# Optimization experiments

Hardware: AMD Instinct MI355X
Metric: run time of the kernel (lower is better)

## Reference

```python
import jax, jax.numpy as jnp
import numpy as np

N_HEAD = 16
N_EMBD = 1024
B, T = 4, 1024


def setup_inputs() -> dict:
    key = jax.random.key(0)
    ks = jax.random.split(key, 8)
    hs = N_EMBD // N_HEAD
    x = jax.random.normal(ks[0], (B, T, N_EMBD), dtype=jnp.float32)
    # previous-layer attention load per token, ~O(1/T) like a softmax column mean
    refractory_state = jax.random.uniform(ks[1], (B, T), dtype=jnp.float32) / T
    s_attn = 1.0 / np.sqrt(N_EMBD)
    W_attn = jax.random.normal(ks[2], (N_EMBD, 3 * N_EMBD), dtype=jnp.float32) * s_attn
    b_attn = jnp.zeros((3 * N_EMBD,), dtype=jnp.float32)
    W_proj = jax.random.normal(ks[3], (N_EMBD, N_EMBD), dtype=jnp.float32) * s_attn
    b_proj = jnp.zeros((N_EMBD,), dtype=jnp.float32)
    # learnable LIF params, init per module (lif_mode='refractory')
    threshold = jnp.full((N_HEAD,), 0.01, dtype=jnp.float32)
    leak = jnp.full((N_HEAD,), 2.0, dtype=jnp.float32)
    steepness = jnp.full((N_HEAD,), 2.0, dtype=jnp.float32)
    ref_strength = jnp.full((N_HEAD,), -2.0, dtype=jnp.float32)
    cross_w = jnp.full((N_HEAD,), -2.0, dtype=jnp.float32)
    return {
        "x": x, "refractory_state": refractory_state,
        "W_attn": W_attn, "b_attn": b_attn,
        "W_proj": W_proj, "b_proj": b_proj,
        "threshold": threshold, "leak": leak, "steepness": steepness,
        "ref_strength": ref_strength, "cross_w": cross_w,
    }


def reference(x, refractory_state, W_attn, b_attn, W_proj, b_proj,
              threshold, leak, steepness, ref_strength, cross_w):
    Bq, Tq, C = x.shape
    H = N_HEAD
    hs = C // H
    qkv = x @ W_attn + b_attn                     # [B,T,3C]
    q, k, v = jnp.split(qkv, 3, axis=-1)
    q = q.reshape(Bq, Tq, H, hs).transpose(0, 2, 1, 3)  # [B,H,T,hs]
    k = k.reshape(Bq, Tq, H, hs).transpose(0, 2, 1, 3)
    v = v.reshape(Bq, Tq, H, hs).transpose(0, 2, 1, 3)

    att = jnp.einsum('bhqd,bhkd->bhqk', q, k) * (1.0 / jnp.sqrt(jnp.asarray(hs, x.dtype)))
    causal = jnp.tril(jnp.ones((Tq, Tq), dtype=bool))
    att = jnp.where(causal[None, None], att, -jnp.inf)
    probs = jax.nn.softmax(att, axis=-1)          # [B,H,T,T]

    thr = (jnp.abs(threshold) * 0.1)[None, :, None, None]
    lk = jax.nn.sigmoid(leak)[None, :, None, None]
    st = jax.nn.softplus(steepness)[None, :, None, None]
    # refractory: column load over queries + cross-layer load
    column_load = probs.mean(axis=-2, keepdims=True)          # [B,H,1,T]
    eff_thr = thr + jax.nn.softplus(ref_strength)[None, :, None, None] * column_load
    eff_thr = eff_thr + jax.nn.sigmoid(cross_w)[None, :, None, None] * refractory_state[:, None, None, :]

    fire = jax.nn.sigmoid(st * (probs - eff_thr))
    lif_w = fire + lk * (1.0 - fire)
    mod = probs * lif_w
    mod = mod / (mod.sum(axis=-1, keepdims=True) + 1e-8)
    new_refractory = mod.mean(axis=1).mean(axis=-2)           # [B,T]

    y = jnp.einsum('bhqk,bhkd->bhqd', mod, v)
    y = y.transpose(0, 2, 1, 3).reshape(Bq, Tq, C)
    y = y @ W_proj + b_proj
    return y, new_refractory
```

## Files before the change

### kernel.cpp

```cpp
#include <hip/hip_runtime.h>
#include <math.h>

#define B_  4
#define T_  1024
#define C_  1024
#define H_  16
#define HS_ 64
#define K2E 0.1803368801f
#define LOG2E 1.44269504f

typedef _Float16 f16;
typedef _Float16 f16x8 __attribute__((ext_vector_type(8)));
typedef _Float16 f16x4 __attribute__((ext_vector_type(4)));
typedef float f32x4 __attribute__((ext_vector_type(4)));

#define MFMA16(a,b,c) __builtin_amdgcn_mfma_f32_16x16x32_f16(a,b,c,0,0,0)
#define EXP2(x) __builtin_amdgcn_exp2f(x)
#define RCP(x)  __builtin_amdgcn_rcpf(x)

#define PSTRIDE_BH 557056

__device__ __forceinline__ float qsum_(float v){
    v += __shfl_xor(v,1,64); v += __shfl_xor(v,2,64);
    v += __shfl_xor(v,4,64); v += __shfl_xor(v,8,64);
    return v;
}
__device__ __forceinline__ float sigmoidf_(float x){ return 1.0f/(1.0f + __expf(-x)); }
__device__ __forceinline__ float softplusf_(float x){ return fmaxf(x, 0.0f) + log1pf(__expf(-fabsf(x))); }

__device__ __forceinline__ void gload_lds16(const f16* g, f16* l){
    __builtin_amdgcn_global_load_lds(
        (__attribute__((address_space(1))) void*)(void*)g,
        (__attribute__((address_space(3))) void*)(void*)l, 16, 0, 0);
}

__global__ __launch_bounds__(256) void prep_k(
    const float* __restrict__ x, const float* __restrict__ Wa,
    const float* __restrict__ Wp,
    f16* __restrict__ x_h, f16* __restrict__ WaT, f16* __restrict__ WpT,
    float* __restrict__ zbase)
{
    __shared__ float tl[32][33];
    const int bid = blockIdx.x, tid = threadIdx.x;
    if (bid < 2048){
        int i = bid*256 + tid;
        const float4* p = (const float4*)x + (size_t)i*2;
        float4 a = p[0], b = p[1];
        f16x8 o;
        o[0]=(f16)a.x; o[1]=(f16)a.y; o[2]=(f16)a.z; o[3]=(f16)a.w;
        o[4]=(f16)b.x; o[5]=(f16)b.y; o[6]=(f16)b.z; o[7]=(f16)b.w;
        *((f16x8*)x_h + i) = o;
    } else if (bid < 5120){
        int t = bid - 2048;
        int n0 = (t % 96)*32, k0 = (t / 96)*32;
        const int c = tid & 31, r4 = tid >> 5;
        #pragma unroll
        for (int i=0;i<4;i++){ int r = r4*4+i; tl[r][c] = Wa[(size_t)(k0+r)*3072 + n0 + c]; }
        __syncthreads();
        #pragma unroll
        for (int i=0;i<4;i++){ int r = r4*4+i; WaT[(size_t)(n0+r)*1024 + k0 + c] = (f16)tl[c][r]; }
    } else if (bid < 6144){
        int t = bid - 5120;
        int n0 = (t & 31)*32, k0 = (t >> 5)*32;
        const int c = tid & 31, r4 = tid >> 5;
        #pragma unroll
        for (int i=0;i<4;i++){ int r = r4*4+i; tl[r][c] = Wp[(size_t)(k0+r)*1024 + n0 + c]; }
        __syncthreads();
        #pragma unroll
        for (int i=0;i<4;i++){ int r = r4*4+i; WpT[(size_t)(n0+r)*1024 + k0 + c] = (f16)tl[c][r]; }
    } else {
        int idx = (bid - 6144)*256 + tid;
        float4 z; z.x=0.f; z.y=0.f; z.z=0.f; z.w=0.f;
        ((float4*)zbase)[idx] = z;
    }
}

#define CT_STRIDE 132
__global__ __launch_bounds__(256) void gemm_qkv_k(
    const f16* __restrict__ A, const f16* __restrict__ Bt,
    const float* __restrict__ bias,
    f16* __restrict__ Qh, f16* __restrict__ Kh, f16* __restrict__ Vt)
{
    __shared__ __align__(16) f16 smem[16896];
    const int tid = threadIdx.x;
    const int lane = tid & 63, wave = tid >> 6;
    const int lx = lane & 15, quad = lane >> 4;
    const int wm = wave & 1, wn = wave >> 1;
    const int lin = blockIdx.y*24 + blockIdx.x;
    const int nb  = (lin & 7)*96 + (lin >> 3);
    const int m0 = (nb/24)*128, n0 = (nb%24)*128;
    const f16* Ap = A  + (size_t)m0*1024;
    const f16* Bp = Bt + (size_t)n0*1024;
    f32x4 acc[4][4];
    #pragma unroll
    for (int i=0;i<4;i++){
        #pragma unroll
        for (int j=0;j<4;j++){ acc[i][j][0]=0.f;acc[i][j][1]=0.f;acc[i][j][2]=0.f;acc[i][j][3]=0.f; }
    }
#define GQ_STAGE(BUF, KT) { \
    const int k0s = (KT)*32; \
    for (int i=0;i<2;i++){ int c=i*4+wave; \
        gload_lds16(Ap + (size_t)(c*16+lx)*1024 + k0s + quad*8, &smem[(BUF) + c*512]); \
        gload_lds16(Bp + (size_t)(c*16+lx)*1024 + k0s + quad*8, &smem[(BUF) + 4096 + c*512]); } }
#define GQ_COMP(BUF) { \
    f16x8 af[4], bf[4]; \
    for (int mt=0;mt<4;mt++) af[mt] = *(const f16x8*)&smem[(BUF) + (wm*4+mt)*512 + quad*128 + lx*8]; \
    for (int nt=0;nt<4;nt++) bf[nt] = *(const f16x8*)&smem[(BUF) + 4096 + (wn*4+nt)*512 + quad*128 + lx*8]; \
    for (int mt=0;mt<4;mt++) \
        for (int nt=0;nt<4;nt++) \
            acc[mt][nt] = MFMA16(af[mt], bf[nt], acc[mt][nt]); }

    GQ_STAGE(0, 0);
    __syncthreads();
    #pragma unroll 1
    for (int it=0; it<32; it+=2){
        if (it+1 < 32) GQ_STAGE(8192, it+1);
        GQ_COMP(0);
        __syncthreads();
        if (it+2 < 32) GQ_STAGE(0, it+2);
        GQ_COMP(8192);
        __syncthreads();
    }
    f16* Ct = smem;
    #pragma unroll
    for (int mt=0;mt<4;mt++){
        #pragma unroll
        for (int nt=0;nt<4;nt++){
            int n_loc = wn*64 + nt*16 + lx;
            float bv = bias[n0 + n_loc];
            #pragma unroll
            for (int r=0;r<4;r++){
                int m_loc = wm*64 + mt*16 + quad*4 + r;
                Ct[m_loc*CT_STRIDE + n_loc] = (f16)(acc[mt][nt][r] + bv);
            }
        }
    }
    __syncthreads();
    const int bb = m0 >> 10;
    if (n0 < 2048){
        for (int it=0; it<8; it++){
            int row = it*32 + wave*8 + (lane>>3);
            int ch  = lane & 7;
            int m_loc = row >> 1, half = row & 1;
            f16x8 v = *(const f16x8*)&Ct[m_loc*CT_STRIDE + half*64 + ch*8];
            int n = n0 + half*64;
            int which = n >> 10, cc = n & 1023, h = cc >> 6;
            int t = (m0 + m_loc) & 1023;
            f16* dst = (which==0) ? Qh : Kh;
            *(f16x8*)(dst + ((size_t)(bb*16+h)*1024 + t)*64 + ch*8) = v;
        }
    } else {
        for (int it=0; it<8; it++){
            int drow = it*16 + wave*4 + (lane>>4);
            int ch   = lane & 15;
            int cc = (n0 + drow) & 1023;
            int h = cc >> 6, d = cc & 63;
            f16 tmp[8];
            #pragma unroll
            for (int j=0;j<8;j++) tmp[j] = Ct[(ch*8+j)*CT_STRIDE + drow];
            int t = (m0 + ch*8) & 1023;
            *(f16x8*)(Vt + ((size_t)(bb*16+h)*64 + d)*1024 + t) = *(f16x8*)tmp;
        }
    }
}

__global__ __launch_bounds__(256) void gemm_proj_k(
    const f16* __restrict__ A, const f16* __restrict__ Bt,
    const float* __restrict__ bias, float* __restrict__ out,
    const float* __restrict__ racc)
{
    if (blockIdx.x == 512){
        float* oref = out + (size_t)B_*T_*C_;
        #pragma unroll
        for (int j=0;j<16;j++){
            int idx = j*256 + threadIdx.x;
            oref[idx] = racc[idx] * (1.0f/(H_*T_));
        }
        return;
    }
    __shared__ __align__(16) f16 smem[12288];
    const int tid = threadIdx.x;
    const int lane = tid & 63, wave = tid >> 6;
    const int lx = lane & 15, quad = lane >> 4;
    const int wm = wave & 1, wn = wave >> 1;
    const int lin = blockIdx.x;
    const int nb  = (lin & 7)*64 + (lin >> 3);
    const int m0 = (nb >> 4)*128, n0 = (nb & 15)*64;
    const f16* Ap = A  + (size_t)m0*1024;
    const f16* Bp = Bt + (size_t)n0*1024;
    f32x4 acc[4][2];
    #pragma unroll
    for (int i=0;i<4;i++){
        #pragma unroll
        for (int j=0;j<2;j++){ acc[i][j][0]=0.f;acc[i][j][1]=0.f;acc[i][j][2]=0.f;acc[i][j][3]=0.f; }
    }
#define GP_STAGE(BUF, KT) { \
    const int k0s = (KT)*32; \
    for (int i=0;i<2;i++){ int c=i*4+wave; \
        gload_lds16(Ap + (size_t)(c*16+lx)*1024 + k0s + quad*8, &smem[(BUF) + c*512]); } \
    gload_lds16(Bp + (size_t)(wave*16+lx)*1024 + k0s + quad*8, &smem[(BUF) + 4096 + wave*512]); }
#define GP_COMP(BUF) { \
    f16x8 af[4], bf[2]; \
    for (int mt=0;mt<4;mt++) af[mt] = *(const f16x8*)&smem[(BUF) + (wm*4+mt)*512 + quad*128 + lx*8]; \
    for (int nt=0;nt<2;nt++) bf[nt] = *(const f16x8*)&smem[(BUF) + 4096 + (wn*2+nt)*512 + quad*128 + lx*8]; \
    for (int mt=0;mt<4;mt++) \
        for (int nt=0;nt<2;nt++) \
            acc[mt][nt] = MFMA16(af[mt], bf[nt], acc[mt][nt]); }

    GP_STAGE(0, 0);
    __syncthreads();
    #pragma unroll 1
    for (int it=0; it<32; it+=2){
        if (it+1 < 32) GP_STAGE(6144, it+1);
        GP_COMP(0);
        __syncthreads();
        if (it+2 < 32) GP_STAGE(0, it+2);
        GP_COMP(6144);
        __syncthreads();
    }
    #pragma unroll
    for (int mt=0;mt<4;mt++){
        #pragma unroll
        for (int nt=0;nt<2;nt++){
            int n = n0 + wn*32 + nt*16 + lx;
            float bv = bias[n];
            #pragma unroll
            for (int r=0;r<4;r++){
                int m = m0 + wm*64 + mt*16 + quad*4 + r;
                out[(size_t)m*1024 + n] = acc[mt][nt][r] + bv;
            }
        }
    }
}

__global__ __launch_bounds__(256) void attn_stats_k(
    const f16* __restrict__ Qh, const f16* __restrict__ Kh,
    float* __restrict__ rowl, float* __restrict__ colp,
    f16* __restrict__ Pbuf)
{
    __shared__ __align__(16) f16 Kl[8192];
    __shared__ __align__(16) f16 Pl[4][16*72];
    __shared__ float invl_sh[64];
    const int tid = threadIdx.x;
    const int lane = tid & 63, wave = tid >> 6;
    const int lx = lane & 15, quad = lane >> 4;
    const int j  = blockIdx.x >> 6;
    const int bh = blockIdx.x & 63;
    const int qpos = wave*16 + quad*4;
    const size_t kbase = (size_t)bh*65536;

#define KLOAD(dst, KT) { \
    for (int i=0;i<2;i++){ int u=i*4+wave, cc=u&3, kh=u>>2; \
        dst[i] = *(const f16x8*)(Kh + kbase + (size_t)((KT)*64 + cc*16+lx)*64 + kh*32 + quad*8); } }
#define KSTORE(src, BUF) { \
    for (int i=0;i<2;i++){ int u=i*4+wave, cc=u&3, kh=u>>2; \
        *(f16x8*)&Kl[(BUF) + cc*1024 + kh*512 + quad*128 + lx*8] = src[i]; } }
#define STATS1_TILE(KT, BUF) { \
    const bool diag = ((KT) == g); \
    for (int nt=0;nt<4;nt++){ \
        f32x4 sc = {0.f,0.f,0.f,0.f}; \
        f16x8 b0 = *(const f16x8*)&Kl[(BUF) + nt*1024 + quad*128 + lx*8]; \
        f16x8 b1 = *(const f16x8*)&Kl[(BUF) + nt*1024 + 512 + quad*128 + lx*8]; \
        sc = MFMA16(aq0, b0, sc); \
        sc = MFMA16(aq1, b1, sc); \
        for (int r=0;r<4;r++){ \
            float sv = sc[r]; \
            if (diag && (nt*16+lx) > (qpos + r)) sv = -1e4f; \
            float p = EXP2(sv*K2E); \
            ls[r] += p; \
            Pl[wave][(quad*4+r)*72 + nt*16 + lx] = (f16)p; \
        } } \
    for (int it2=0; it2<2; it2++){ \
        int qq = it2*8 + (lane>>3), chh = lane & 7; \
        f16x8 v = *(const f16x8*)&Pl[wave][qq*72 + chh*8]; \
        *(f16x8*)(Pblk + (size_t)(wave*16+qq)*S + (KT)*64 + chh*8) = v; } }

    #pragma unroll 1
    for (int pass=0; pass<2; ++pass){
        const int g = pass ? j : (15 - j);
        const int S = (g+1)*64;
        f16* __restrict__ Pblk = Pbuf + (size_t)bh*PSTRIDE_BH + (size_t)4096*((g*(g+1))>>1);
        const size_t qoff = ((size_t)bh*1024 + g*64 + wave*16 + lx)*64;
        f16x8 aq0 = *(const f16x8*)(Qh + qoff + quad*8);
        f16x8 aq1 = *(const f16x8*)(Qh + qoff + 32 + quad*8);

        f16x8 rkE[2], rkO[2];
        float ls[4] = {0.f,0.f,0.f,0.f};
        KLOAD(rkE, 0);
        KSTORE(rkE, 0);
        if (g >= 1) KLOAD(rkO, 1);
        __syncthreads();
        #pragma unroll 1
        for (int kt=0; kt<=g; kt+=2){
            if (kt+2 <= g) KLOAD(rkE, kt+2);
            if (kt+1 <= g) KSTORE(rkO, 4096);
            STATS1_TILE(kt, 0);
            __syncthreads();
            if (kt+1 <= g){
                if (kt+3 <= g) KLOAD(rkO, kt+3);
                if (kt+2 <= g) KSTORE(rkE, 0);
                STATS1_TILE(kt+1, 4096);
                __syncthreads();
            }
        }
        #pragma unroll
        for (int r=0;r<4;r++){
            float l = qsum_(ls[r]);
            if (lx == 0){
                rowl[(size_t)bh*1024 + g*64 + qpos + r] = l;
                invl_sh[qpos + r] = RCP(l);
            }
        }
        __syncthreads();
        if (tid < (g+1)*16){
            const int k0 = tid*4;
            float a0=0.f, a1=0.f, a2=0.f, a3=0.f;
            const f16* pr = Pblk + k0;
            #pragma unroll 4
            for (int q=0;q<64;q++){
                f16x4 v = *(const f16x4*)(pr + (size_t)q*S);
                float w = invl_sh[q];
                a0 += (float)v[0]*w; a1 += (float)v[1]*w;
                a2 += (float)v[2]*w; a3 += (float)v[3]*w;
            }
            float* cp = colp + (size_t)bh*1024 + k0;
            atomicAdd(cp+0,a0); atomicAdd(cp+1,a1);
            atomicAdd(cp+2,a2); atomicAdd(cp+3,a3);
        }
    }
}

__global__ __launch_bounds__(256) void attn_apply_k(
    const f16* __restrict__ Vt,
    const float* __restrict__ rowl,
    const float* __restrict__ colp, const float* __restrict__ refr,
    const float* __restrict__ threshold, const float* __restrict__ leak,
    const float* __restrict__ steepness, const float* __restrict__ ref_strength,
    const float* __restrict__ cross_w,
    f16* __restrict__ Yh, float* __restrict__ racc,
    f16* __restrict__ Pbuf)
{
    __shared__ __align__(16) f16 Vl[8192];
    __shared__ __align__(16) f16 Pl[4][16*72];
    __shared__ float eb[1024];
    __shared__ float invl_sh[64];
    __shared__ float invD_sh[64];
    const int tid = threadIdx.x;
    const int lane = tid & 63, wave = tid >> 6;
    const int lx = lane & 15, quad = lane >> 4;
    const int qr8 = lane >> 3, c8 = lane & 7;
    const int j  = blockIdx.x >> 6;
    const int bh = blockIdx.x & 63;
    const int b  = bh >> 4, h = bh & 15;
    const size_t kbase = (size_t)bh*65536;

    const float thr = fabsf(threshold[h])*0.1f;
    const float lk  = sigmoidf_(leak[h]);
    const float st2 = softplusf_(steepness[h]) * LOG2E;
    const float sprT= softplusf_(ref_strength[h]) * (1.0f/T_);
    const float cw  = sigmoidf_(cross_w[h]);
    const float Alk = 1.f - lk;

    {
        float4 cp = *(const float4*)(colp + (size_t)bh*1024 + tid*4);
        float4 rf = *(const float4*)(refr + (size_t)b*1024 + tid*4);
        eb[tid*4+0] = st2*(thr + sprT*cp.x + cw*rf.x);
        eb[tid*4+1] = st2*(thr + sprT*cp.y + cw*rf.y);
        eb[tid*4+2] = st2*(thr + sprT*cp.z + cw*rf.z);
        eb[tid*4+3] = st2*(thr + sprT*cp.w + cw*rf.w);
    }

#define VLOAD(dst, KT) { \
    for (int i=0;i<2;i++){ int u=i*4+wave, cc=u&3, kh=u>>2; \
        dst[i] = *(const f16x8*)(Vt + kbase + (size_t)(cc*16+lx)*1024 + (KT)*64 + kh*32 + quad*8); } }
#define VSTORE(src, BUF) { \
    for (int i=0;i<2;i++){ int u=i*4+wave, cc=u&3, kh=u>>2; \
        *(f16x8*)&Vl[(BUF) + cc*1024 + kh*512 + quad*128 + lx*8] = src[i]; } }
#define PLOAD(dst, KT) { \
    dst[0] = *(const f16x8*)(Pblk + (size_t)(wave*16 + qr8)*S + (KT)*64 + c8*8); \
    dst[1] = *(const f16x8*)(Pblk + (size_t)(wave*16 + 8 + qr8)*S + (KT)*64 + c8*8); }
#define APPLY1_TILE(KT, BUF, pv) { \
    float ebv[8]; \
    *(float4*)&ebv[0] = *(const float4*)&eb[(KT)*64 + c8*8]; \
    *(float4*)&ebv[4] = *(const float4*)&eb[(KT)*64 + c8*8 + 4]; \
    f16x8 o0, o1; \
    for (int jj=0;jj<8;jj++){ \
        float pj = (float)pv[0][jj] * w0; \
        float fire = RCP(1.f + EXP2(ebv[jj] - st2*pj)); \
        float pw = pj*(lk + Alk*fire); \
        Dp0 += pw; o0[jj] = (f16)pw; } \
    for (int jj=0;jj<8;jj++){ \
        float pj = (float)pv[1][jj] * w1; \
        float fire = RCP(1.f + EXP2(ebv[jj] - st2*pj)); \
        float pw = pj*(lk + Alk*fire); \
        Dp1 += pw; o1[jj] = (f16)pw; } \
    *(f16x8*)&Pl[wave][qr8*72 + c8*8] = o0; \
    *(f16x8*)&Pl[wave][(8+qr8)*72 + c8*8] = o1; \
    { f16x8 ap0 = *(const f16x8*)&Pl[wave][lx*72 + quad*8]; \
      f16x8 ap1 = *(const f16x8*)&Pl[wave][lx*72 + 32 + quad*8]; \
      for (int dt=0;dt<4;dt++){ \
        f16x8 bv0 = *(const f16x8*)&Vl[(BUF) + dt*1024 + quad*128 + lx*8]; \
        f16x8 bv1 = *(const f16x8*)&Vl[(BUF) + dt*1024 + 512 + quad*128 + lx*8]; \
        y[dt] = MFMA16(ap0, bv0, y[dt]); \
        y[dt] = MFMA16(ap1, bv1, y[dt]); } } }

    #pragma unroll 1
    for (int pass=0; pass<2; ++pass){
        const int g = pass ? j : (15 - j);
        const int S = (g+1)*64;
        f16* __restrict__ Pblk = Pbuf + (size_t)bh*PSTRIDE_BH + (size_t)4096*((g*(g+1))>>1);

        __syncthreads();
        if (tid < 64) invl_sh[tid] = RCP(rowl[(size_t)bh*1024 + g*64 + tid]);
        __syncthreads();

        const float w0 = invl_sh[wave*16 + qr8];
        const float w1 = invl_sh[wave*16 + 8 + qr8];

        f32x4 y[4];
        #pragma unroll
        for (int i=0;i<4;i++){ y[i][0]=0.f;y[i][1]=0.f;y[i][2]=0.f;y[i][3]=0.f; }
        float Dp0 = 0.f, Dp1 = 0.f;

        f16x8 rvE[2], rvO[2], pvE[2], pvO[2];
        VLOAD(rvE, 0); PLOAD(pvE, 0);
        VSTORE(rvE, 0);
        if (g >= 1){ VLOAD(rvO, 1); PLOAD(pvO, 1); }
        __syncthreads();
        #pragma unroll 1
        for (int kt=0; kt<=g; kt+=2){
            if (kt+2 <= g) VLOAD(rvE, kt+2);
            if (kt+1 <= g) VSTORE(rvO, 4096);
            APPLY1_TILE(kt, 0, pvE);
            if (kt+2 <= g) PLOAD(pvE, kt+2);
            __syncthreads();
            if (kt+1 <= g){
                if (kt+3 <= g) VLOAD(rvO, kt+3);
                if (kt+2 <= g) VSTORE(rvE, 0);
                APPLY1_TILE(kt+1, 4096, pvO);
                if (kt+3 <= g) PLOAD(pvO, kt+3);
                __syncthreads();
            }
        }
        Dp0 += __shfl_xor(Dp0,1,64); Dp0 += __shfl_xor(Dp0,2,64); Dp0 += __shfl_xor(Dp0,4,64);
        Dp1 += __shfl_xor(Dp1,1,64); Dp1 += __shfl_xor(Dp1,2,64); Dp1 += __shfl_xor(Dp1,4,64);
        if (c8 == 0){
            invD_sh[wave*16 + qr8]     = RCP(Dp0 + 1e-8f);
            invD_sh[wave*16 + 8 + qr8] = RCP(Dp1 + 1e-8f);
        }
        __syncthreads();

        float invD[4];
        #pragma unroll
        for (int r=0;r<4;r++) invD[r] = invD_sh[wave*16 + quad*4 + r];
        #pragma unroll
        for (int dt=0;dt<4;dt++){
            #pragma unroll
            for (int r=0;r<4;r++)
                Pl[wave][(quad*4+r)*72 + dt*16 + lx] = (f16)(y[dt][r]*invD[r]);
        }
        #pragma unroll
        for (int it=0; it<2; it++){
            int q = it*8 + (lane>>3), ch = lane & 7;
            f16x8 v = *(const f16x8*)&Pl[wave][q*72 + ch*8];
            *(f16x8*)(Yh + (size_t)(b*1024 + g*64 + wave*16 + q)*1024 + h*64 + ch*8) = v;
        }

        if (tid < (g+1)*16){
            const int k0 = tid*4;
            float4 ebv = *(const float4*)&eb[k0];
            float a0=0.f, a1=0.f, a2=0.f, a3=0.f;
            const f16* pr = Pblk + k0;
            #pragma unroll 4
            for (int q=0;q<64;q++){
                f16x4 v = *(const f16x4*)(pr + (size_t)q*S);
                float wl = invl_sh[q], wd = invD_sh[q];
                float p0 = (float)v[0]*wl, p1 = (float)v[1]*wl;
                float p2 = (float)v[2]*wl, p3 = (float)v[3]*wl;
                float f0 = RCP(1.f + EXP2(ebv.x - st2*p0));
                float f1 = RCP(1.f + EXP2(ebv.y - st2*p1));
                float f2 = RCP(1.f + EXP2(ebv.z - st2*p2));
                float f3 = RCP(1.f + EXP2(ebv.w - st2*p3));
                a0 += p0*(lk + Alk*f0)*wd; a1 += p1*(lk + Alk*f1)*wd;
                a2 += p2*(lk + Alk*f2)*wd; a3 += p3*(lk + Alk*f3)*wd;
            }
            float* rp = racc + (size_t)b*1024 + k0;
            atomicAdd(rp+0,a0); atomicAdd(rp+1,a1);
            atomicAdd(rp+2,a2); atomicAdd(rp+3,a3);
        }
    }
}

extern "C" void kernel_launch(void* const* d_in, const int* in_sizes, int n_in,
                              void* d_out, int out_size, void* d_ws, size_t ws_size,
                              hipStream_t stream) {
    (void)in_sizes; (void)n_in; (void)out_size; (void)ws_size;
    const float* x           = (const float*)d_in[0];
    const float* refr        = (const float*)d_in[1];
    const float* W_attn      = (const float*)d_in[2];
    const float* b_attn      = (const float*)d_in[3];
    const float* W_proj      = (const float*)d_in[4];
    const float* b_proj      = (const float*)d_in[5];
    const float* threshold   = (const float*)d_in[6];
    const float* leak        = (const float*)d_in[7];
    const float* steepness   = (const float*)d_in[8];
    const float* ref_strength= (const float*)d_in[9];
    const float* cross_w     = (const float*)d_in[10];
    float* out = (float*)d_out;

    char* ws = (char*)d_ws;
    f16* x_h = (f16*)ws;                       ws += (size_t)4096*1024*2;
    f16* WaT = (f16*)ws;                       ws += (size_t)3072*1024*2;
    f16* WpT = (f16*)ws;                       ws += (size_t)1024*1024*2;
    f16* Qh  = (f16*)ws;                       ws += (size_t)64*1024*64*2;
    f16* Kh  = (f16*)ws;                       ws += (size_t)64*1024*64*2;
    f16* Vt  = (f16*)ws;                       ws += (size_t)64*64*1024*2;
    f16* Yh  = (f16*)ws;                       ws += (size_t)4096*1024*2;
    float* rowl = (float*)ws;                  ws += (size_t)65536*4;
    float* colp = (float*)ws;                  ws += (size_t)65536*4;
    float* racc = (float*)ws;                  ws += (size_t)4096*4;
    f16* Pbuf = (f16*)ws;                      ws += (size_t)64*PSTRIDE_BH*2;

    prep_k<<<dim3(6212), dim3(256), 0, stream>>>(x, W_attn, W_proj, x_h, WaT, WpT, colp);
    gemm_qkv_k<<<dim3(24,32), dim3(256), 0, stream>>>(x_h, WaT, b_attn, Qh, Kh, Vt);
    attn_stats_k<<<dim3(512), dim3(256), 0, stream>>>(Qh, Kh, rowl, colp, Pbuf);
    attn_apply_k<<<dim3(512), dim3(256), 0, stream>>>(
        Vt, rowl, colp, refr,
        threshold, leak, steepness, ref_strength, cross_w, Yh, racc, Pbuf);
    gemm_proj_k<<<dim3(513), dim3(256), 0, stream>>>(Yh, WpT, b_proj, out, racc);
}
```

Baseline: 268.8 us.

## Split paired query tiles into separate blocks and load K/V directly into registers

Both attention kernels used to process two query tiles per block (g and 15-g) to balance causal work. Now each block handles a single tile, with twice as many blocks launched, ordered so the heaviest tiles start first. The K and V tiles are no longer staged through shared memory. Each wave loads its MFMA B operands straight from global memory into registers, which removes the LDS stores and most __syncthreads in the main loops. The cost is redundant global and L2 reads across the four waves, more registers, and reliance on block scheduling for load balance.

```diff
diff --git a/kernel.cpp b/kernel.cpp
--- a/kernel.cpp
+++ b/kernel.cpp
@@ -238,31 +238,33 @@
     float* __restrict__ rowl, float* __restrict__ colp,
     f16* __restrict__ Pbuf)
 {
-    __shared__ __align__(16) f16 Kl[8192];
     __shared__ __align__(16) f16 Pl[4][16*72];
     __shared__ float invl_sh[64];
     const int tid = threadIdx.x;
     const int lane = tid & 63, wave = tid >> 6;
     const int lx = lane & 15, quad = lane >> 4;
-    const int j  = blockIdx.x >> 6;
+    const int g  = 15 - (blockIdx.x >> 6);
     const int bh = blockIdx.x & 63;
     const int qpos = wave*16 + quad*4;
     const size_t kbase = (size_t)bh*65536;
-
-#define KLOAD(dst, KT) { \
-    for (int i=0;i<2;i++){ int u=i*4+wave, cc=u&3, kh=u>>2; \
-        dst[i] = *(const f16x8*)(Kh + kbase + (size_t)((KT)*64 + cc*16+lx)*64 + kh*32 + quad*8); } }
-#define KSTORE(src, BUF) { \
-    for (int i=0;i<2;i++){ int u=i*4+wave, cc=u&3, kh=u>>2; \
-        *(f16x8*)&Kl[(BUF) + cc*1024 + kh*512 + quad*128 + lx*8] = src[i]; } }
-#define STATS1_TILE(KT, BUF) { \
+    const int S = (g+1)*64;
+    f16* __restrict__ Pblk = Pbuf + (size_t)bh*PSTRIDE_BH + (size_t)4096*((g*(g+1))>>1);
+
+    const size_t qoff = ((size_t)bh*1024 + g*64 + wave*16 + lx)*64;
+    f16x8 aq0 = *(const f16x8*)(Qh + qoff + quad*8);
+    f16x8 aq1 = *(const f16x8*)(Qh + qoff + 32 + quad*8);
+
+#define KLOADX(dst, KT) { \
+    for (int nt=0;nt<4;nt++){ \
+        const f16* kp = Kh + kbase + (size_t)((KT)*64 + nt*16 + lx)*64 + quad*8; \
+        dst[nt*2]   = *(const f16x8*)(kp); \
+        dst[nt*2+1] = *(const f16x8*)(kp + 32); } }
+#define STATS_TILE(KT, rk) { \
     const bool diag = ((KT) == g); \
     for (int nt=0;nt<4;nt++){ \
         f32x4 sc = {0.f,0.f,0.f,0.f}; \
-        f16x8 b0 = *(const f16x8*)&Kl[(BUF) + nt*1024 + quad*128 + lx*8]; \
-        f16x8 b1 = *(const f16x8*)&Kl[(BUF) + nt*1024 + 512 + quad*128 + lx*8]; \
-        sc = MFMA16(aq0, b0, sc); \
-        sc = MFMA16(aq1, b1, sc); \
+        sc = MFMA16(aq0, rk[nt*2],   sc); \
+        sc = MFMA16(aq1, rk[nt*2+1], sc); \
         for (int r=0;r<4;r++){ \
             float sv = sc[r]; \
             if (diag && (nt*16+lx) > (qpos + r)) sv = -1e4f; \
@@ -275,58 +277,42 @@
         f16x8 v = *(const f16x8*)&Pl[wave][qq*72 + chh*8]; \
         *(f16x8*)(Pblk + (size_t)(wave*16+qq)*S + (KT)*64 + chh*8) = v; } }
 
+    f16x8 rkE[8], rkO[8];
+    float ls[4] = {0.f,0.f,0.f,0.f};
+    KLOADX(rkE, 0);
+    if (g >= 1) KLOADX(rkO, 1);
     #pragma unroll 1
-    for (int pass=0; pass<2; ++pass){
-        const int g = pass ? j : (15 - j);
-        const int S = (g+1)*64;
-        f16* __restrict__ Pblk = Pbuf + (size_t)bh*PSTRIDE_BH + (size_t)4096*((g*(g+1))>>1);
-        const size_t qoff = ((size_t)bh*1024 + g*64 + wave*16 + lx)*64;
-        f16x8 aq0 = *(const f16x8*)(Qh + qoff + quad*8);
-        f16x8 aq1 = *(const f16x8*)(Qh + qoff + 32 + quad*8);
-
-        f16x8 rkE[2], rkO[2];
-        float ls[4] = {0.f,0.f,0.f,0.f};
-        KLOAD(rkE, 0);
-        KSTORE(rkE, 0);
-        if (g >= 1) KLOAD(rkO, 1);
-        __syncthreads();
-        #pragma unroll 1
-        for (int kt=0; kt<=g; kt+=2){
-            if (kt+2 <= g) KLOAD(rkE, kt+2);
-            if (kt+1 <= g) KSTORE(rkO, 4096);
-            STATS1_TILE(kt, 0);
-            __syncthreads();
-            if (kt+1 <= g){
-                if (kt+3 <= g) KLOAD(rkO, kt+3);
-                if (kt+2 <= g) KSTORE(rkE, 0);
-                STATS1_TILE(kt+1, 4096);
-                __syncthreads();
-            }
-        }
-        #pragma unroll
-        for (int r=0;r<4;r++){
-            float l = qsum_(ls[r]);
-            if (lx == 0){
-                rowl[(size_t)bh*1024 + g*64 + qpos + r] = l;
-                invl_sh[qpos + r] = RCP(l);
-            }
-        }
-        __syncthreads();
-        if (tid < (g+1)*16){
-            const int k0 = tid*4;
-            float a0=0.f, a1=0.f, a2=0.f, a3=0.f;
-            const f16* pr = Pblk + k0;
-            #pragma unroll 4
-            for (int q=0;q<64;q++){
-                f16x4 v = *(const f16x4*)(pr + (size_t)q*S);
-                float w = invl_sh[q];
-                a0 += (float)v[0]*w; a1 += (float)v[1]*w;
-                a2 += (float)v[2]*w; a3 += (float)v[3]*w;
-            }
-            float* cp = colp + (size_t)bh*1024 + k0;
-            atomicAdd(cp+0,a0); atomicAdd(cp+1,a1);
-            atomicAdd(cp+2,a2); atomicAdd(cp+3,a3);
-        }
+    for (int kt=0; kt<=g; kt+=2){
+        STATS_TILE(kt, rkE);
+        if (kt+2 <= g) KLOADX(rkE, kt+2);
+        if (kt+1 <= g){
+            STATS_TILE(kt+1, rkO);
+            if (kt+3 <= g) KLOADX(rkO, kt+3);
+        }
+    }
+    #pragma unroll
+    for (int r=0;r<4;r++){
+        float l = qsum_(ls[r]);
+        if (lx == 0){
+            rowl[(size_t)bh*1024 + g*64 + qpos + r] = l;
+            invl_sh[qpos + r] = RCP(l);
+        }
+    }
+    __syncthreads();
+    if (tid < (g+1)*16){
+        const int k0 = tid*4;
+        float a0=0.f, a1=0.f, a2=0.f, a3=0.f;
+        const f16* pr = Pblk + k0;
+        #pragma unroll 4
+        for (int q=0;q<64;q++){
+            f16x4 v = *(const f16x4*)(pr + (size_t)q*S);
+            float w = invl_sh[q];
+            a0 += (float)v[0]*w; a1 += (float)v[1]*w;
+            a2 += (float)v[2]*w; a3 += (float)v[3]*w;
+        }
+        float* cp = colp + (size_t)bh*1024 + k0;
+        atomicAdd(cp+0,a0); atomicAdd(cp+1,a1);
+        atomicAdd(cp+2,a2); atomicAdd(cp+3,a3);
     }
 }
 
@@ -340,7 +326,6 @@
     f16* __restrict__ Yh, float* __restrict__ racc,
     f16* __restrict__ Pbuf)
 {
-    __shared__ __align__(16) f16 Vl[8192];
     __shared__ __align__(16) f16 Pl[4][16*72];
     __shared__ float eb[1024];
     __shared__ float invl_sh[64];
@@ -348,11 +333,12 @@
     const int tid = threadIdx.x;
     const int lane = tid & 63, wave = tid >> 6;
     const int lx = lane & 15, quad = lane >> 4;
-    const int qr8 = lane >> 3, c8 = lane & 7;
-    const int j  = blockIdx.x >> 6;
+    const int g  = 15 - (blockIdx.x >> 6);
     const int bh = blockIdx.x & 63;
     const int b  = bh >> 4, h = bh & 15;
     const size_t kbase = (size_t)bh*65536;
+    const int S = (g+1)*64;
+    f16* __restrict__ Pblk = Pbuf + (size_t)bh*PSTRIDE_BH + (size_t)4096*((g*(g+1))>>1);
 
     const float thr = fabsf(threshold[h])*0.1f;
     const float lk  = sigmoidf_(leak[h]);
@@ -369,125 +355,107 @@
         eb[tid*4+2] = st2*(thr + sprT*cp.z + cw*rf.z);
         eb[tid*4+3] = st2*(thr + sprT*cp.w + cw*rf.w);
     }
-
-#define VLOAD(dst, KT) { \
-    for (int i=0;i<2;i++){ int u=i*4+wave, cc=u&3, kh=u>>2; \
-        dst[i] = *(const f16x8*)(Vt + kbase + (size_t)(cc*16+lx)*1024 + (KT)*64 + kh*32 + quad*8); } }
-#define VSTORE(src, BUF) { \
-    for (int i=0;i<2;i++){ int u=i*4+wave, cc=u&3, kh=u>>2; \
-        *(f16x8*)&Vl[(BUF) + cc*1024 + kh*512 + quad*128 + lx*8] = src[i]; } }
-#define PLOAD(dst, KT) { \
-    dst[0] = *(const f16x8*)(Pblk + (size_t)(wave*16 + qr8)*S + (KT)*64 + c8*8); \
-    dst[1] = *(const f16x8*)(Pblk + (size_t)(wave*16 + 8 + qr8)*S + (KT)*64 + c8*8); }
-#define APPLY1_TILE(KT, BUF, pv) { \
-    float ebv[8]; \
-    *(float4*)&ebv[0] = *(const float4*)&eb[(KT)*64 + c8*8]; \
-    *(float4*)&ebv[4] = *(const float4*)&eb[(KT)*64 + c8*8 + 4]; \
-    f16x8 o0, o1; \
+    if (tid < 64) invl_sh[tid] = RCP(rowl[(size_t)bh*1024 + g*64 + tid]);
+    __syncthreads();
+
+    const float wli = invl_sh[wave*16 + lx];
+
+    f32x4 y[4];
+    #pragma unroll
+    for (int i=0;i<4;i++){ y[i][0]=0.f;y[i][1]=0.f;y[i][2]=0.f;y[i][3]=0.f; }
+    float Dp = 0.f;
+
+#define PLOADX(dst, KT) { \
+    const f16* pp = Pblk + (size_t)(wave*16 + lx)*S + (KT)*64 + quad*8; \
+    dst[0] = *(const f16x8*)(pp); \
+    dst[1] = *(const f16x8*)(pp + 32); }
+#define RVLOAD(dst, KT) { \
+    for (int dt=0;dt<4;dt++){ \
+        const f16* vp = Vt + kbase + (size_t)(dt*16 + lx)*1024 + (KT)*64 + quad*8; \
+        dst[dt*2]   = *(const f16x8*)(vp); \
+        dst[dt*2+1] = *(const f16x8*)(vp + 32); } }
+#define LIF_TILE(KT, pv, af0, af1) { \
+    const float* ebp = &eb[(KT)*64 + quad*8]; \
+    float4 eA0 = *(const float4*)(ebp); \
+    float4 eA1 = *(const float4*)(ebp+4); \
+    float4 eB0 = *(const float4*)(ebp+32); \
+    float4 eB1 = *(const float4*)(ebp+36); \
+    float ea[8] = {eA0.x,eA0.y,eA0.z,eA0.w,eA1.x,eA1.y,eA1.z,eA1.w}; \
+    float ebb[8] = {eB0.x,eB0.y,eB0.z,eB0.w,eB1.x,eB1.y,eB1.z,eB1.w}; \
     for (int jj=0;jj<8;jj++){ \
-        float pj = (float)pv[0][jj] * w0; \
-        float fire = RCP(1.f + EXP2(ebv[jj] - st2*pj)); \
-        float pw = pj*(lk + Alk*fire); \
-        Dp0 += pw; o0[jj] = (f16)pw; } \
+        float p = (float)pv[0][jj] * wli; \
+        float fire = RCP(1.f + EXP2(ea[jj] - st2*p)); \
+        float pw = p*(lk + Alk*fire); \
+        Dp += pw; af0[jj] = (f16)pw; } \
     for (int jj=0;jj<8;jj++){ \
-        float pj = (float)pv[1][jj] * w1; \
-        float fire = RCP(1.f + EXP2(ebv[jj] - st2*pj)); \
-        float pw = pj*(lk + Alk*fire); \
-        Dp1 += pw; o1[jj] = (f16)pw; } \
-    *(f16x8*)&Pl[wave][qr8*72 + c8*8] = o0; \
-    *(f16x8*)&Pl[wave][(8+qr8)*72 + c8*8] = o1; \
-    { f16x8 ap0 = *(const f16x8*)&Pl[wave][lx*72 + quad*8]; \
-      f16x8 ap1 = *(const f16x8*)&Pl[wave][lx*72 + 32 + quad*8]; \
-      for (int dt=0;dt<4;dt++){ \
-        f16x8 bv0 = *(const f16x8*)&Vl[(BUF) + dt*1024 + quad*128 + lx*8]; \
-        f16x8 bv1 = *(const f16x8*)&Vl[(BUF) + dt*1024 + 512 + quad*128 + lx*8]; \
-        y[dt] = MFMA16(ap0, bv0, y[dt]); \
-        y[dt] = MFMA16(ap1, bv1, y[dt]); } } }
-
+        float p = (float)pv[1][jj] * wli; \
+        float fire = RCP(1.f + EXP2(ebb[jj] - st2*p)); \
+        float pw = p*(lk + Alk*fire); \
+        Dp += pw; af1[jj] = (f16)pw; } }
+#define MFMA8(af0, af1, rv) { \
+    for (int dt=0;dt<4;dt++){ \
+        y[dt] = MFMA16(af0, rv[dt*2],   y[dt]); \
+        y[dt] = MFMA16(af1, rv[dt*2+1], y[dt]); } }
+
+    f16x8 rv[8], pvE[2], pvO[2], af0, af1;
+    PLOADX(pvE, 0);
+    if (g >= 1) PLOADX(pvO, 1);
     #pragma unroll 1
-    for (int pass=0; pass<2; ++pass){
-        const int g = pass ? j : (15 - j);
-        const int S = (g+1)*64;
-        f16* __restrict__ Pblk = Pbuf + (size_t)bh*PSTRIDE_BH + (size_t)4096*((g*(g+1))>>1);
-
-        __syncthreads();
-        if (tid < 64) invl_sh[tid] = RCP(rowl[(size_t)bh*1024 + g*64 + tid]);
-        __syncthreads();
-
-        const float w0 = invl_sh[wave*16 + qr8];
-        const float w1 = invl_sh[wave*16 + 8 + qr8];
-
-        f32x4 y[4];
-        #pragma unroll
-        for (int i=0;i<4;i++){ y[i][0]=0.f;y[i][1]=0.f;y[i][2]=0.f;y[i][3]=0.f; }
-        float Dp0 = 0.f, Dp1 = 0.f;
-
-        f16x8 rvE[2], rvO[2], pvE[2], pvO[2];
-        VLOAD(rvE, 0); PLOAD(pvE, 0);
-        VSTORE(rvE, 0);
-        if (g >= 1){ VLOAD(rvO, 1); PLOAD(pvO, 1); }
-        __syncthreads();
-        #pragma unroll 1
-        for (int kt=0; kt<=g; kt+=2){
-            if (kt+2 <= g) VLOAD(rvE, kt+2);
-            if (kt+1 <= g) VSTORE(rvO, 4096);
-            APPLY1_TILE(kt, 0, pvE);
-            if (kt+2 <= g) PLOAD(pvE, kt+2);
-            __syncthreads();
-            if (kt+1 <= g){
-                if (kt+3 <= g) VLOAD(rvO, kt+3);
-                if (kt+2 <= g) VSTORE(rvE, 0);
-                APPLY1_TILE(kt+1, 4096, pvO);
-                if (kt+3 <= g) PLOAD(pvO, kt+3);
-                __syncthreads();
-            }
-        }
-        Dp0 += __shfl_xor(Dp0,1,64); Dp0 += __shfl_xor(Dp0,2,64); Dp0 += __shfl_xor(Dp0,4,64);
-        Dp1 += __shfl_xor(Dp1,1,64); Dp1 += __shfl_xor(Dp1,2,64); Dp1 += __shfl_xor(Dp1,4,64);
-        if (c8 == 0){
-            invD_sh[wave*16 + qr8]     = RCP(Dp0 + 1e-8f);
-            invD_sh[wave*16 + 8 + qr8] = RCP(Dp1 + 1e-8f);
-        }
-        __syncthreads();
-
-        float invD[4];
-        #pragma unroll
-        for (int r=0;r<4;r++) invD[r] = invD_sh[wave*16 + quad*4 + r];
-        #pragma unroll
-        for (int dt=0;dt<4;dt++){
-            #pragma unroll
-            for (int r=0;r<4;r++)
-                Pl[wave][(quad*4+r)*72 + dt*16 + lx] = (f16)(y[dt][r]*invD[r]);
-        }
-        #pragma unroll
-        for (int it=0; it<2; it++){
-            int q = it*8 + (lane>>3), ch = lane & 7;
-            f16x8 v = *(const f16x8*)&Pl[wave][q*72 + ch*8];
-            *(f16x8*)(Yh + (size_t)(b*1024 + g*64 + wave*16 + q)*1024 + h*64 + ch*8) = v;
-        }
-
-        if (tid < (g+1)*16){
-            const int k0 = tid*4;
-            float4 ebv = *(const float4*)&eb[k0];
-            float a0=0.f, a1=0.f, a2=0.f, a3=0.f;
-            const f16* pr = Pblk + k0;
-            #pragma unroll 4
-            for (int q=0;q<64;q++){
-                f16x4 v = *(const f16x4*)(pr + (size_t)q*S);
-                float wl = invl_sh[q], wd = invD_sh[q];
-                float p0 = (float)v[0]*wl, p1 = (float)v[1]*wl;
-                float p2 = (float)v[2]*wl, p3 = (float)v[3]*wl;
-                float f0 = RCP(1.f + EXP2(ebv.x - st2*p0));
-                float f1 = RCP(1.f + EXP2(ebv.y - st2*p1));
-                float f2 = RCP(1.f + EXP2(ebv.z - st2*p2));
-                float f3 = RCP(1.f + EXP2(ebv.w - st2*p3));
-                a0 += p0*(lk + Alk*f0)*wd; a1 += p1*(lk + Alk*f1)*wd;
-                a2 += p2*(lk + Alk*f2)*wd; a3 += p3*(lk + Alk*f3)*wd;
-            }
-            float* rp = racc + (size_t)b*1024 + k0;
-            atomicAdd(rp+0,a0); atomicAdd(rp+1,a1);
-            atomicAdd(rp+2,a2); atomicAdd(rp+3,a3);
-        }
+    for (int kt=0; kt<=g; kt+=2){
+        RVLOAD(rv, kt);
+        LIF_TILE(kt, pvE, af0, af1);
+        if (kt+2 <= g) PLOADX(pvE, kt+2);
+        MFMA8(af0, af1, rv);
+        if (kt+1 <= g){
+            RVLOAD(rv, kt+1);
+            LIF_TILE(kt+1, pvO, af0, af1);
+            if (kt+3 <= g) PLOADX(pvO, kt+3);
+            MFMA8(af0, af1, rv);
+        }
+    }
+    Dp += __shfl_xor(Dp,16,64); Dp += __shfl_xor(Dp,32,64);
+    float invDl = RCP(Dp + 1e-8f);
+    if (quad == 0) invD_sh[wave*16 + lx] = invDl;
+
+    float invD[4];
+    #pragma unroll
+    for (int r=0;r<4;r++) invD[r] = invD_sh[wave*16 + quad*4 + r];
+    #pragma unroll
+    for (int dt=0;dt<4;dt++){
+        #pragma unroll
+        for (int r=0;r<4;r++)
+            Pl[wave][(quad*4+r)*72 + dt*16 + lx] = (f16)(y[dt][r]*invD[r]);
+    }
+    #pragma unroll
+    for (int it=0; it<2; it++){
+        int q = it*8 + (lane>>3), ch = lane & 7;
+        f16x8 v = *(const f16x8*)&Pl[wave][q*72 + ch*8];
+        *(f16x8*)(Yh + (size_t)(b*1024 + g*64 + wave*16 + q)*1024 + h*64 + ch*8) = v;
+    }
+
+    __syncthreads();
+
+    if (tid < (g+1)*16){
+        const int k0 = tid*4;
+        float4 ebv = *(const float4*)&eb[k0];
+        float a0=0.f, a1=0.f, a2=0.f, a3=0.f;
+        const f16* pr = Pblk + k0;
+        #pragma unroll 4
+        for (int q=0;q<64;q++){
+            f16x4 v = *(const f16x4*)(pr + (size_t)q*S);
+            float wl = invl_sh[q], wd = invD_sh[q];
+            float p0 = (float)v[0]*wl, p1 = (float)v[1]*wl;
+            float p2 = (float)v[2]*wl, p3 = (float)v[3]*wl;
+            float f0 = RCP(1.f + EXP2(ebv.x - st2*p0));
+            float f1 = RCP(1.f + EXP2(ebv.y - st2*p1));
+            float f2 = RCP(1.f + EXP2(ebv.z - st2*p2));
+            float f3 = RCP(1.f + EXP2(ebv.w - st2*p3));
+            a0 += p0*(lk + Alk*f0)*wd; a1 += p1*(lk + Alk*f1)*wd;
+            a2 += p2*(lk + Alk*f2)*wd; a3 += p3*(lk + Alk*f3)*wd;
+        }
+        float* rp = racc + (size_t)b*1024 + k0;
+        atomicAdd(rp+0,a0); atomicAdd(rp+1,a1);
+        atomicAdd(rp+2,a2); atomicAdd(rp+3,a3);
     }
 }
 
@@ -523,8 +491,8 @@
 
     prep_k<<<dim3(6212), dim3(256), 0, stream>>>(x, W_attn, W_proj, x_h, WaT, WpT, colp);
     gemm_qkv_k<<<dim3(24,32), dim3(256), 0, stream>>>(x_h, WaT, b_attn, Qh, Kh, Vt);
-    attn_stats_k<<<dim3(512), dim3(256), 0, stream>>>(Qh, Kh, rowl, colp, Pbuf);
-    attn_apply_k<<<dim3(512), dim3(256), 0, stream>>>(
+    attn_stats_k<<<dim3(1024), dim3(256), 0, stream>>>(Qh, Kh, rowl, colp, Pbuf);
+    attn_apply_k<<<dim3(1024), dim3(256), 0, stream>>>(
         Vt, rowl, colp, refr,
         threshold, leak, steepness, ref_strength, cross_w, Yh, racc, Pbuf);
     gemm_proj_k<<<dim3(513), dim3(256), 0, stream>>>(Yh, WpT, b_proj, out, racc);
```

Result: slower. 293.0 us (+9.0%).
